# Kernel optimization log

Measured on AMD Instinct MI355X. Metric: run time of the kernel, lower is better.

Reference implementation:

```python
import jax, jax.numpy as jnp
import numpy as np

B, C, N = 4, 256, 4096
OUT = 256
TEMP = OUT ** 0.5  # temperature = sqrt(out_channel)


def setup_inputs() -> dict:
    key = jax.random.key(0)
    kx, kxx, kq, kk, kv = jax.random.split(key, 5)
    x = jax.random.normal(kx, (B, C, N), dtype=jnp.float32)
    xx = jax.random.normal(kxx, (B, C, N), dtype=jnp.float32)
    # Conv1d(in, out, kernel=1, bias=False) weights, squeezed to (out, in)
    s = 1.0 / np.sqrt(C)
    Wq = jax.random.uniform(kq, (OUT, C), jnp.float32, -s, s)
    Wk = jax.random.uniform(kk, (OUT, C), jnp.float32, -s, s)
    Wv = jax.random.uniform(kv, (OUT, C), jnp.float32, -s, s)
    return {"x": x, "xx": xx, "Wq": Wq, "Wk": Wk, "Wv": Wv}


def reference(x, xx, Wq, Wk, Wv):
    # 1x1 conv == per-point linear: (out,in) x (b,in,n) -> (b,out,n)
    q = jnp.einsum('oc,bcn->bon', Wq, x)
    k = jnp.einsum('oc,bcn->bon', Wk, xx)
    v = jnp.einsum('oc,bcn->bon', Wv, xx)
    # attn = (q^T / temp) @ k : (B, N, N)
    attn = jax.nn.softmax(jnp.einsum('bon,bom->bnm', q, k) / TEMP, axis=-1)
    # dropout is identity in eval mode
    # y = attn @ v^T -> (B, N, OUT); returned transposed to (B, OUT, N)
    y = jnp.einsum('bnm,bom->bon', attn, v)
    return y
```

## Files before the change

### kernel.cpp

```cpp
#include <hip/hip_runtime.h>
#include <hip/hip_bf16.h>


typedef __attribute__((ext_vector_type(8))) short bf16x8;
typedef __attribute__((ext_vector_type(4))) float f32x4;
typedef __attribute__((ext_vector_type(4))) short short4t;

constexpr int B_ = 4;
constexpr int C_ = 256;
constexpr int N_ = 4096;
constexpr int O_ = 256;
constexpr float INV_TEMP = 1.0f / 16.0f;
constexpr int SPLIT = 2;
constexpr int MCHUNK = N_ / SPLIT;
constexpr int NITER = MCHUNK / 64;

__device__ __forceinline__ short f2bf(float f) {
  union { float f; unsigned u; } v; v.f = f;
  unsigned r = v.u + 0x7fffu + ((v.u >> 16) & 1u);
  return (short)(r >> 16);
}

__device__ __forceinline__ void dma16(const short* g, short* l) {
  __builtin_amdgcn_global_load_lds(
      (const __attribute__((address_space(1))) unsigned int*)g,
      (__attribute__((address_space(3))) unsigned int*)l, 16, 0, 0);
}

__global__ void wcvt(const float* __restrict__ Wq, const float* __restrict__ Wk,
                     const float* __restrict__ Wv, short* __restrict__ wb) {
  int i = blockIdx.x * 256 + threadIdx.x;
  int mat = i >> 16, off = i & 65535;
  const float* W = (mat == 0) ? Wq : (mat == 1 ? Wk : Wv);
  wb[i] = f2bf(W[off]);
}

__global__ void zero_k(float4* __restrict__ out4, float4* __restrict__ lp4) {
  int i = blockIdx.x * 256 + threadIdx.x;
  if (i < 1048576) out4[i] = (float4){0.f, 0.f, 0.f, 0.f};
  else lp4[i - 1048576] = (float4){0.f, 0.f, 0.f, 0.f};
}

__global__ void norm_k(float* __restrict__ out, const float* __restrict__ lp) {
  int i = blockIdx.x * 256 + threadIdx.x;
  int e = i * 4;
  int n = e & (N_ - 1);
  int b = e >> 20;
  float4 o = ((float4*)out)[i];
  const float4 l = *(const float4*)&lp[(b << 12) + n];
  o.x /= l.x; o.y /= l.y; o.z /= l.z; o.w /= l.w;
  ((float4*)out)[i] = o;
}

__global__ __launch_bounds__(256, 2) void qkv_proj(
    const float* __restrict__ x, const float* __restrict__ xx,
    const short* __restrict__ wb,
    short* __restrict__ qg, short* __restrict__ kt, short* __restrict__ vt) {
  const int n0  = blockIdx.x * 64;
  const int b   = blockIdx.y;
  const int mat = blockIdx.z;
  const float* src = (mat == 0) ? x : xx;
  const short* W   = wb + mat * 65536;
  const int tid = threadIdx.x;
  const int w = tid >> 6, lane = tid & 63;
  const int g = lane >> 4, c16 = lane & 15;

  __shared__ short xs[64][264];

  {
    const int n = tid & 63, cq = tid >> 6;
    const float* sp = src + (size_t)b * C_ * N_ + n0 + n;
#pragma unroll
    for (int rep = 0; rep < 16; ++rep) {
      int c = rep * 16 + cq * 4;
      short4t s4;
#pragma unroll
      for (int j = 0; j < 4; ++j) s4[j] = f2bf(sp[(size_t)(c + j) * N_]);
      *(short4t*)&xs[n][c] = s4;
    }
  }
  __syncthreads();

  f32x4 acc[4][4];
#pragma unroll
  for (int i = 0; i < 4; ++i)
#pragma unroll
    for (int j = 0; j < 4; ++j) acc[i][j] = (f32x4){0.f, 0.f, 0.f, 0.f};

#pragma unroll
  for (int ko = 0; ko < 8; ++ko) {
    bf16x8 wfr[4], xfr[4];
#pragma unroll
    for (int ot = 0; ot < 4; ++ot)
      wfr[ot] = *(const bf16x8*)&W[(w * 64 + ot * 16 + c16) * C_ + ko * 32 + g * 8];
#pragma unroll
    for (int nt = 0; nt < 4; ++nt)
      xfr[nt] = *(const bf16x8*)&xs[nt * 16 + c16][ko * 32 + g * 8];
    if (mat < 2) {
#pragma unroll
      for (int ot = 0; ot < 4; ++ot)
#pragma unroll
        for (int nt = 0; nt < 4; ++nt)
          acc[ot][nt] = __builtin_amdgcn_mfma_f32_16x16x32_bf16(
              wfr[ot], xfr[nt], acc[ot][nt], 0, 0, 0);
    } else {
#pragma unroll
      for (int mt = 0; mt < 4; ++mt)
#pragma unroll
        for (int ot = 0; ot < 4; ++ot)
          acc[mt][ot] = __builtin_amdgcn_mfma_f32_16x16x32_bf16(
              xfr[mt], wfr[ot], acc[mt][ot], 0, 0, 0);
    }
  }

  if (mat == 0) {
    short* dst = qg + (size_t)b * N_ * O_;
#pragma unroll
    for (int ot = 0; ot < 4; ++ot)
#pragma unroll
      for (int nt = 0; nt < 4; ++nt) {
        int n = n0 + nt * 16 + c16;
        int o = w * 64 + ot * 16 + g * 4;
        short4t s;
        s[0] = f2bf(acc[ot][nt][0] * INV_TEMP);
        s[1] = f2bf(acc[ot][nt][1] * INV_TEMP);
        s[2] = f2bf(acc[ot][nt][2] * INV_TEMP);
        s[3] = f2bf(acc[ot][nt][3] * INV_TEMP);
        *(short4t*)(dst + (size_t)n * O_ + o) = s;
      }
  } else if (mat == 1) {
#pragma unroll
    for (int ot = 0; ot < 4; ++ot)
#pragma unroll
      for (int nt = 0; nt < 4; ++nt) {
        int m = n0 + nt * 16 + c16;
        int o0 = w * 64 + ot * 16 + g * 4;
        int koo = o0 >> 5;
        int pos = ((o0 & 31) >> 3) ^ ((c16 >> 1) & 3);
        size_t base =
            (((size_t)(b * 256 + (m >> 4)) * 8 + koo) * 16 + c16) * 32 +
            pos * 8 + (g & 1) * 4;
        short4t s;
        s[0] = f2bf(acc[ot][nt][0]);
        s[1] = f2bf(acc[ot][nt][1]);
        s[2] = f2bf(acc[ot][nt][2]);
        s[3] = f2bf(acc[ot][nt][3]);
        *(short4t*)(kt + base) = s;
      }
  } else {
#pragma unroll
    for (int mt = 0; mt < 4; ++mt)
#pragma unroll
      for (int ot = 0; ot < 4; ++ot) {
        int o = w * 64 + ot * 16 + c16;
        int mloc = mt * 16 + g * 4;
        int chunk = mloc >> 3;
        int pos = chunk ^ (o & 7);
        size_t base =
            ((size_t)(b * 64 + (n0 >> 6)) * 256 + o) * 64 + pos * 8 + (g & 1) * 4;
        short4t s;
        s[0] = f2bf(acc[mt][ot][0]);
        s[1] = f2bf(acc[mt][ot][1]);
        s[2] = f2bf(acc[mt][ot][2]);
        s[3] = f2bf(acc[mt][ot][3]);
        *(short4t*)(vt + base) = s;
      }
  }
}

__global__ __launch_bounds__(256, 2) void flash_attn(
    const short* __restrict__ qg, const short* __restrict__ kt,
    const short* __restrict__ vt, float* __restrict__ out,
    float* __restrict__ lp) {
  const int n0 = blockIdx.x * 64;
  const int b  = blockIdx.y;
  const int mbase = blockIdx.z * MCHUNK;
  const int tid = threadIdx.x;
  const int w = tid >> 6, lane = tid & 63;
  const int g = lane >> 4, c16 = lane & 15;

  __shared__ short kb[16384];
  __shared__ short vb[16384];
  __shared__ short ps[64][72];

  const short* ktb = kt + (size_t)b * N_ * O_;
  const short* vtb = vt + (size_t)b * N_ * O_;

  bf16x8 qf[4][8];
#pragma unroll
  for (int nt = 0; nt < 4; ++nt) {
    const short* qrow =
        qg + (size_t)(b * N_ + n0 + nt * 16 + c16) * O_ + g * 8;
#pragma unroll
    for (int ko = 0; ko < 8; ++ko) qf[nt][ko] = *(const bf16x8*)(qrow + ko * 32);
  }

  f32x4 oacc[4][4];
#pragma unroll
  for (int i = 0; i < 4; ++i)
#pragma unroll
    for (int j = 0; j < 4; ++j) oacc[i][j] = (f32x4){0.f, 0.f, 0.f, 0.f};
  float lrun[4] = {0.f, 0.f, 0.f, 0.f};

  {
    const short* src = ktb + ((size_t)(mbase >> 4) + w) * 4096;
#pragma unroll
    for (int j = 0; j < 8; ++j)
      dma16(src + j * 512 + lane * 8, &kb[w * 4096 + j * 512]);
  }
  __syncthreads();

  const int sw = (g ^ ((c16 >> 1) & 3)) * 8;

  for (int mi = 0; mi < NITER; ++mi) {
    {
      const short* src = vtb + ((size_t)(mbase >> 6) + mi) * 16384 + w * 4096;
#pragma unroll
      for (int j = 0; j < 8; ++j)
        dma16(src + j * 512 + lane * 8, &vb[w * 4096 + j * 512]);
    }

    f32x4 sacc[4];
#pragma unroll
    for (int nt = 0; nt < 4; ++nt) sacc[nt] = (f32x4){0.f, 0.f, 0.f, 0.f};
#pragma unroll
    for (int ko = 0; ko < 8; ++ko) {
      bf16x8 kf = *(const bf16x8*)&kb[w * 4096 + (ko * 16 + c16) * 32 + sw];
#pragma unroll
      for (int nt = 0; nt < 4; ++nt)
        sacc[nt] = __builtin_amdgcn_mfma_f32_16x16x32_bf16(
            kf, qf[nt][ko], sacc[nt], 0, 0, 0);
    }

#pragma unroll
    for (int nt = 0; nt < 4; ++nt) {
      short4t pb;
      float rs = 0.f;
#pragma unroll
      for (int r = 0; r < 4; ++r) {
        float p = __expf(sacc[nt][r]);
        rs += p;
        pb[r] = f2bf(p);
      }
      lrun[nt] += rs;
      *(short4t*)&ps[nt * 16 + c16][w * 16 + g * 4] = pb;
    }

    __syncthreads();

    if (mi + 1 < NITER) {
      const short* src =
          ktb + ((size_t)(mbase >> 4) + (mi + 1) * 4 + w) * 4096;
#pragma unroll
      for (int j = 0; j < 8; ++j)
        dma16(src + j * 512 + lane * 8, &kb[w * 4096 + j * 512]);
    }

#pragma unroll
    for (int kk = 0; kk < 2; ++kk) {
      bf16x8 pf[4];
#pragma unroll
      for (int nt = 0; nt < 4; ++nt)
        pf[nt] = *(const bf16x8*)&ps[nt * 16 + c16][kk * 32 + g * 8];
#pragma unroll
      for (int ot = 0; ot < 4; ++ot) {
        int pos = (kk * 4 + g) ^ (c16 & 7);
        bf16x8 vf =
            *(const bf16x8*)&vb[(w * 64 + ot * 16 + c16) * 64 + pos * 8];
#pragma unroll
        for (int nt = 0; nt < 4; ++nt)
          oacc[ot][nt] = __builtin_amdgcn_mfma_f32_16x16x32_bf16(
              vf, pf[nt], oacc[ot][nt], 0, 0, 0);
      }
    }

    __syncthreads();
  }

#pragma unroll
  for (int nt = 0; nt < 4; ++nt) {
    float v = lrun[nt];
    v += __shfl_xor(v, 16);
    v += __shfl_xor(v, 32);
    if (lane < 16) atomicAdd(&lp[(b << 12) + n0 + nt * 16 + lane], v);
  }

#pragma unroll
  for (int ot = 0; ot < 4; ++ot)
#pragma unroll
    for (int nt = 0; nt < 4; ++nt) {
      const int n = n0 + nt * 16 + c16;
      float* op = out + (size_t)b * O_ * N_ +
                  (size_t)(w * 64 + ot * 16 + g * 4) * N_ + n;
#pragma unroll
      for (int r = 0; r < 4; ++r)
        atomicAdd(op + (size_t)r * N_, oacc[ot][nt][r]);
    }
}

extern "C" void kernel_launch(void* const* d_in, const int* in_sizes, int n_in,
                              void* d_out, int out_size, void* d_ws,
                              size_t ws_size, hipStream_t stream) {
  const float* x  = (const float*)d_in[0];
  const float* xx = (const float*)d_in[1];
  const float* Wq = (const float*)d_in[2];
  const float* Wk = (const float*)d_in[3];
  const float* Wv = (const float*)d_in[4];
  float* out = (float*)d_out;

  short* qg = (short*)d_ws;
  short* kt = qg + (size_t)B_ * N_ * O_;
  short* vt = kt + (size_t)B_ * N_ * O_;
  float* lp = (float*)(vt + (size_t)B_ * N_ * O_);
  short* wb = (short*)(lp + B_ * N_);

  wcvt<<<768, 256, 0, stream>>>(Wq, Wk, Wv, wb);
  zero_k<<<4112, 256, 0, stream>>>((float4*)out, (float4*)lp);
  qkv_proj<<<dim3(N_ / 64, B_, 3), 256, 0, stream>>>(x, xx, wb, qg, kt, vt);
  flash_attn<<<dim3(64, B_, SPLIT), 256, 0, stream>>>(qg, kt, vt, out, lp);
  norm_k<<<4096, 256, 0, stream>>>(out, lp);
}
```

Before: 209.2 us.

## Warp-specialize flash attention, drop key split, atomics, zero and normalize kernels

Flash attention now runs 512-thread blocks where four producer waves compute QK^T and exp into double-buffered P tiles while four consumer waves load V and accumulate PV one step behind. The key-split and its atomics, the zeroing kernel and the separate normalization kernel are removed; row sums go through shared memory and the output is normalized and stored directly. The projection kernel stages its output tile in LDS so global writes are coalesced. This halves the grid, to 256 blocks, and doubles LDS use per block, which may limit occupancy and load balance.

```diff
diff --git a/kernel.cpp b/kernel.cpp
--- a/kernel.cpp
+++ b/kernel.cpp
@@ -11,9 +11,7 @@
 constexpr int N_ = 4096;
 constexpr int O_ = 256;
 constexpr float INV_TEMP = 1.0f / 16.0f;
-constexpr int SPLIT = 2;
-constexpr int MCHUNK = N_ / SPLIT;
-constexpr int NITER = MCHUNK / 64;
+constexpr int NIT = 64;
 
 __device__ __forceinline__ short f2bf(float f) {
   union { float f; unsigned u; } v; v.f = f;
@@ -33,23 +31,6 @@
   int mat = i >> 16, off = i & 65535;
   const float* W = (mat == 0) ? Wq : (mat == 1 ? Wk : Wv);
   wb[i] = f2bf(W[off]);
-}
-
-__global__ void zero_k(float4* __restrict__ out4, float4* __restrict__ lp4) {
-  int i = blockIdx.x * 256 + threadIdx.x;
-  if (i < 1048576) out4[i] = (float4){0.f, 0.f, 0.f, 0.f};
-  else lp4[i - 1048576] = (float4){0.f, 0.f, 0.f, 0.f};
-}
-
-__global__ void norm_k(float* __restrict__ out, const float* __restrict__ lp) {
-  int i = blockIdx.x * 256 + threadIdx.x;
-  int e = i * 4;
-  int n = e & (N_ - 1);
-  int b = e >> 20;
-  float4 o = ((float4*)out)[i];
-  const float4 l = *(const float4*)&lp[(b << 12) + n];
-  o.x /= l.x; o.y /= l.y; o.z /= l.z; o.w /= l.w;
-  ((float4*)out)[i] = o;
 }
 
 __global__ __launch_bounds__(256, 2) void qkv_proj(
@@ -65,7 +46,7 @@
   const int w = tid >> 6, lane = tid & 63;
   const int g = lane >> 4, c16 = lane & 15;
 
-  __shared__ short xs[64][264];
+  __shared__ __align__(16) short xs[64][264];
 
   {
     const int n = tid & 63, cq = tid >> 6;
@@ -113,39 +94,36 @@
     }
   }
 
+  __syncthreads();
+  short* ob = &xs[0][0];
+
   if (mat == 0) {
-    short* dst = qg + (size_t)b * N_ * O_;
 #pragma unroll
     for (int ot = 0; ot < 4; ++ot)
 #pragma unroll
       for (int nt = 0; nt < 4; ++nt) {
-        int n = n0 + nt * 16 + c16;
-        int o = w * 64 + ot * 16 + g * 4;
+        int f = (nt * 16 + c16) * 256 + w * 64 + ot * 16 + g * 4;
         short4t s;
         s[0] = f2bf(acc[ot][nt][0] * INV_TEMP);
         s[1] = f2bf(acc[ot][nt][1] * INV_TEMP);
         s[2] = f2bf(acc[ot][nt][2] * INV_TEMP);
         s[3] = f2bf(acc[ot][nt][3] * INV_TEMP);
-        *(short4t*)(dst + (size_t)n * O_ + o) = s;
+        *(short4t*)&ob[f] = s;
       }
   } else if (mat == 1) {
 #pragma unroll
     for (int ot = 0; ot < 4; ++ot)
 #pragma unroll
       for (int nt = 0; nt < 4; ++nt) {
-        int m = n0 + nt * 16 + c16;
-        int o0 = w * 64 + ot * 16 + g * 4;
-        int koo = o0 >> 5;
-        int pos = ((o0 & 31) >> 3) ^ ((c16 >> 1) & 3);
-        size_t base =
-            (((size_t)(b * 256 + (m >> 4)) * 8 + koo) * 16 + c16) * 32 +
-            pos * 8 + (g & 1) * 4;
+        int koo = w * 2 + (ot >> 1);
+        int pos = (((ot & 1) * 2 + (g >> 1)) ^ ((c16 >> 1) & 3));
+        int f = nt * 4096 + koo * 512 + c16 * 32 + pos * 8 + (g & 1) * 4;
         short4t s;
         s[0] = f2bf(acc[ot][nt][0]);
         s[1] = f2bf(acc[ot][nt][1]);
         s[2] = f2bf(acc[ot][nt][2]);
         s[3] = f2bf(acc[ot][nt][3]);
-        *(short4t*)(kt + base) = s;
+        *(short4t*)&ob[f] = s;
       }
   } else {
 #pragma unroll
@@ -153,149 +131,167 @@
 #pragma unroll
       for (int ot = 0; ot < 4; ++ot) {
         int o = w * 64 + ot * 16 + c16;
-        int mloc = mt * 16 + g * 4;
-        int chunk = mloc >> 3;
-        int pos = chunk ^ (o & 7);
-        size_t base =
-            ((size_t)(b * 64 + (n0 >> 6)) * 256 + o) * 64 + pos * 8 + (g & 1) * 4;
+        int pos = (mt * 2 + (g >> 1)) ^ (o & 7);
+        int f = o * 64 + pos * 8 + (g & 1) * 4;
         short4t s;
         s[0] = f2bf(acc[mt][ot][0]);
         s[1] = f2bf(acc[mt][ot][1]);
         s[2] = f2bf(acc[mt][ot][2]);
         s[3] = f2bf(acc[mt][ot][3]);
-        *(short4t*)(vt + base) = s;
-      }
-  }
-}
-
-__global__ __launch_bounds__(256, 2) void flash_attn(
+        *(short4t*)&ob[f] = s;
+      }
+  }
+  __syncthreads();
+
+  short* dst = (mat == 0) ? qg + ((size_t)b * N_ + n0) * O_
+             : (mat == 1) ? kt + (size_t)(b * 256 + (n0 >> 4)) * 4096
+                          : vt + (size_t)(b * 64 + (n0 >> 6)) * 16384;
+  const uint4* s4 = (const uint4*)ob;
+  uint4* d4 = (uint4*)dst;
+#pragma unroll
+  for (int j = 0; j < 8; ++j) d4[j * 256 + tid] = s4[j * 256 + tid];
+}
+
+__global__ __launch_bounds__(512, 2) void flash_attn(
     const short* __restrict__ qg, const short* __restrict__ kt,
-    const short* __restrict__ vt, float* __restrict__ out,
-    float* __restrict__ lp) {
-  const int n0 = blockIdx.x * 64;
-  const int b  = blockIdx.y;
-  const int mbase = blockIdx.z * MCHUNK;
+    const short* __restrict__ vt, float* __restrict__ out) {
+  const int xg = blockIdx.x;
+  const int b  = xg >> 1;
+  const int n0 = (((xg & 1) << 5) + blockIdx.y) * 64;
   const int tid = threadIdx.x;
   const int w = tid >> 6, lane = tid & 63;
   const int g = lane >> 4, c16 = lane & 15;
-
-  __shared__ short kb[16384];
-  __shared__ short vb[16384];
-  __shared__ short ps[64][72];
+  const bool prod = (w < 4);
+  const int pw = w & 3;
+
+  __shared__ short kb[2][16384];
+  __shared__ short vb[2][16384];
+  __shared__ short ps[2][64][72];
+  __shared__ float lsum[4][64];
 
   const short* ktb = kt + (size_t)b * N_ * O_;
   const short* vtb = vt + (size_t)b * N_ * O_;
 
   bf16x8 qf[4][8];
-#pragma unroll
-  for (int nt = 0; nt < 4; ++nt) {
-    const short* qrow =
-        qg + (size_t)(b * N_ + n0 + nt * 16 + c16) * O_ + g * 8;
-#pragma unroll
-    for (int ko = 0; ko < 8; ++ko) qf[nt][ko] = *(const bf16x8*)(qrow + ko * 32);
-  }
-
+  float lrun[4] = {0.f, 0.f, 0.f, 0.f};
   f32x4 oacc[4][4];
 #pragma unroll
   for (int i = 0; i < 4; ++i)
 #pragma unroll
     for (int j = 0; j < 4; ++j) oacc[i][j] = (f32x4){0.f, 0.f, 0.f, 0.f};
-  float lrun[4] = {0.f, 0.f, 0.f, 0.f};
-
-  {
-    const short* src = ktb + ((size_t)(mbase >> 4) + w) * 4096;
+
+  if (prod) {
+#pragma unroll
+    for (int nt = 0; nt < 4; ++nt) {
+      const short* qrow =
+          qg + (size_t)(b * N_ + n0 + nt * 16 + c16) * O_ + g * 8;
+#pragma unroll
+      for (int ko = 0; ko < 8; ++ko)
+        qf[nt][ko] = *(const bf16x8*)(qrow + ko * 32);
+    }
+    const short* src = ktb + (size_t)pw * 4096;
 #pragma unroll
     for (int j = 0; j < 8; ++j)
-      dma16(src + j * 512 + lane * 8, &kb[w * 4096 + j * 512]);
+      dma16(src + j * 512 + lane * 8, &kb[0][pw * 4096 + j * 512]);
   }
   __syncthreads();
 
   const int sw = (g ^ ((c16 >> 1) & 3)) * 8;
 
-  for (int mi = 0; mi < NITER; ++mi) {
-    {
-      const short* src = vtb + ((size_t)(mbase >> 6) + mi) * 16384 + w * 4096;
-#pragma unroll
-      for (int j = 0; j < 8; ++j)
-        dma16(src + j * 512 + lane * 8, &vb[w * 4096 + j * 512]);
-    }
-
-    f32x4 sacc[4];
-#pragma unroll
-    for (int nt = 0; nt < 4; ++nt) sacc[nt] = (f32x4){0.f, 0.f, 0.f, 0.f};
-#pragma unroll
-    for (int ko = 0; ko < 8; ++ko) {
-      bf16x8 kf = *(const bf16x8*)&kb[w * 4096 + (ko * 16 + c16) * 32 + sw];
-#pragma unroll
-      for (int nt = 0; nt < 4; ++nt)
-        sacc[nt] = __builtin_amdgcn_mfma_f32_16x16x32_bf16(
-            kf, qf[nt][ko], sacc[nt], 0, 0, 0);
-    }
-
+  for (int i = 0; i <= NIT; ++i) {
+    if (prod) {
+      if (i < NIT) {
+        if (i + 1 < NIT) {
+          const short* src = ktb + (size_t)(4 * (i + 1) + pw) * 4096;
+          short* dst = &kb[(i + 1) & 1][pw * 4096];
+#pragma unroll
+          for (int j = 0; j < 8; ++j)
+            dma16(src + j * 512 + lane * 8, dst + j * 512);
+        }
+        const short* ksl = &kb[i & 1][pw * 4096];
+        f32x4 sacc[4];
+#pragma unroll
+        for (int nt = 0; nt < 4; ++nt) sacc[nt] = (f32x4){0.f, 0.f, 0.f, 0.f};
+#pragma unroll
+        for (int ko = 0; ko < 8; ++ko) {
+          bf16x8 kf = *(const bf16x8*)&ksl[(ko * 16 + c16) * 32 + sw];
+#pragma unroll
+          for (int nt = 0; nt < 4; ++nt)
+            sacc[nt] = __builtin_amdgcn_mfma_f32_16x16x32_bf16(
+                kf, qf[nt][ko], sacc[nt], 0, 0, 0);
+        }
+#pragma unroll
+        for (int nt = 0; nt < 4; ++nt) {
+          short4t pb;
+          float rs = 0.f;
+#pragma unroll
+          for (int r = 0; r < 4; ++r) {
+            float p = __expf(sacc[nt][r]);
+            rs += p;
+            pb[r] = f2bf(p);
+          }
+          lrun[nt] += rs;
+          *(short4t*)&ps[i & 1][nt * 16 + c16][pw * 16 + g * 4] = pb;
+        }
+      }
+    } else {
+      if (i < NIT) {
+        const short* src = vtb + (size_t)i * 16384 + pw * 4096;
+        short* dst = &vb[i & 1][pw * 4096];
+#pragma unroll
+        for (int j = 0; j < 8; ++j)
+          dma16(src + j * 512 + lane * 8, dst + j * 512);
+      }
+      if (i > 0) {
+        const int pb_ = (i - 1) & 1;
+#pragma unroll
+        for (int kk = 0; kk < 2; ++kk) {
+          bf16x8 pf[4];
+#pragma unroll
+          for (int nt = 0; nt < 4; ++nt)
+            pf[nt] = *(const bf16x8*)&ps[pb_][nt * 16 + c16][kk * 32 + g * 8];
+#pragma unroll
+          for (int ot = 0; ot < 4; ++ot) {
+            int pos = (kk * 4 + g) ^ (c16 & 7);
+            bf16x8 vf = *(const bf16x8*)
+                &vb[pb_][(pw * 64 + ot * 16 + c16) * 64 + pos * 8];
+#pragma unroll
+            for (int nt = 0; nt < 4; ++nt)
+              oacc[ot][nt] = __builtin_amdgcn_mfma_f32_16x16x32_bf16(
+                  vf, pf[nt], oacc[ot][nt], 0, 0, 0);
+          }
+        }
+      }
+    }
+    __syncthreads();
+  }
+
+  if (prod) {
 #pragma unroll
     for (int nt = 0; nt < 4; ++nt) {
-      short4t pb;
-      float rs = 0.f;
-#pragma unroll
-      for (int r = 0; r < 4; ++r) {
-        float p = __expf(sacc[nt][r]);
-        rs += p;
-        pb[r] = f2bf(p);
-      }
-      lrun[nt] += rs;
-      *(short4t*)&ps[nt * 16 + c16][w * 16 + g * 4] = pb;
-    }
-
-    __syncthreads();
-
-    if (mi + 1 < NITER) {
-      const short* src =
-          ktb + ((size_t)(mbase >> 4) + (mi + 1) * 4 + w) * 4096;
-#pragma unroll
-      for (int j = 0; j < 8; ++j)
-        dma16(src + j * 512 + lane * 8, &kb[w * 4096 + j * 512]);
-    }
-
-#pragma unroll
-    for (int kk = 0; kk < 2; ++kk) {
-      bf16x8 pf[4];
-#pragma unroll
-      for (int nt = 0; nt < 4; ++nt)
-        pf[nt] = *(const bf16x8*)&ps[nt * 16 + c16][kk * 32 + g * 8];
+      float v = lrun[nt];
+      v += __shfl_xor(v, 16);
+      v += __shfl_xor(v, 32);
+      if (lane < 16) lsum[pw][nt * 16 + lane] = v;
+    }
+  }
+  __syncthreads();
+  if (!prod) {
+#pragma unroll
+    for (int nt = 0; nt < 4; ++nt) {
+      const int nl = nt * 16 + c16;
+      float l = lsum[0][nl] + lsum[1][nl] + lsum[2][nl] + lsum[3][nl];
+      float li = 1.0f / l;
 #pragma unroll
       for (int ot = 0; ot < 4; ++ot) {
-        int pos = (kk * 4 + g) ^ (c16 & 7);
-        bf16x8 vf =
-            *(const bf16x8*)&vb[(w * 64 + ot * 16 + c16) * 64 + pos * 8];
-#pragma unroll
-        for (int nt = 0; nt < 4; ++nt)
-          oacc[ot][nt] = __builtin_amdgcn_mfma_f32_16x16x32_bf16(
-              vf, pf[nt], oacc[ot][nt], 0, 0, 0);
-      }
-    }
-
-    __syncthreads();
-  }
-
-#pragma unroll
-  for (int nt = 0; nt < 4; ++nt) {
-    float v = lrun[nt];
-    v += __shfl_xor(v, 16);
-    v += __shfl_xor(v, 32);
-    if (lane < 16) atomicAdd(&lp[(b << 12) + n0 + nt * 16 + lane], v);
-  }
-
-#pragma unroll
-  for (int ot = 0; ot < 4; ++ot)
-#pragma unroll
-    for (int nt = 0; nt < 4; ++nt) {
-      const int n = n0 + nt * 16 + c16;
-      float* op = out + (size_t)b * O_ * N_ +
-                  (size_t)(w * 64 + ot * 16 + g * 4) * N_ + n;
-#pragma unroll
-      for (int r = 0; r < 4; ++r)
-        atomicAdd(op + (size_t)r * N_, oacc[ot][nt][r]);
-    }
+        float* op = out + ((size_t)b * O_ + pw * 64 + ot * 16 + g * 4) * N_ +
+                    n0 + nl;
+#pragma unroll
+        for (int r = 0; r < 4; ++r)
+          op[(size_t)r * N_] = oacc[ot][nt][r] * li;
+      }
+    }
+  }
 }
 
 extern "C" void kernel_launch(void* const* d_in, const int* in_sizes, int n_in,
@@ -311,12 +307,9 @@
   short* qg = (short*)d_ws;
   short* kt = qg + (size_t)B_ * N_ * O_;
   short* vt = kt + (size_t)B_ * N_ * O_;
-  float* lp = (float*)(vt + (size_t)B_ * N_ * O_);
-  short* wb = (short*)(lp + B_ * N_);
+  short* wb = vt + (size_t)B_ * N_ * O_;
 
   wcvt<<<768, 256, 0, stream>>>(Wq, Wk, Wv, wb);
-  zero_k<<<4112, 256, 0, stream>>>((float4*)out, (float4*)lp);
   qkv_proj<<<dim3(N_ / 64, B_, 3), 256, 0, stream>>>(x, xx, wb, qg, kt, vt);
-  flash_attn<<<dim3(64, B_, SPLIT), 256, 0, stream>>>(qg, kt, vt, out, lp);
-  norm_k<<<4096, 256, 0, stream>>>(out, lp);
-}
+  flash_attn<<<dim3(8, 32), 512, 0, stream>>>(qg, kt, vt, out);
+}
```

Result: no change. 207.3 us (-0.9%).
